# Kernel tuning notes

Measured on AMD Instinct MI355X. Metric: run time of the kernel, lower is better.

## Reference

```python
import jax, jax.numpy as jnp
import numpy as np

LN_EPS = 1e-5

def setup_inputs() -> dict:
    key = jax.random.key(0)
    ks = jax.random.split(key, 5)
    B, S, Dv, Dl, V = 4, 576, 1024, 4096, 32000
    return {
        "vision_feats": jax.random.normal(ks[0], (B, S, Dv), dtype=jnp.float32),
        "W1_w": jax.random.normal(ks[1], (Dl, Dv), dtype=jnp.float32) * (Dv ** -0.5),
        "W1_b": jax.random.normal(ks[2], (Dl,), dtype=jnp.float32) * 0.02,
        "W2_w": jax.random.normal(ks[3], (V, Dl), dtype=jnp.float32) * (Dl ** -0.5),
        "llm_token_embed": jax.random.normal(ks[4], (V, Dl), dtype=jnp.float32) * 0.02,
    }

def reference(vision_feats, W1_w, W1_b, W2_w, llm_token_embed):
    # W1: (B,S,Dv) @ (Dv,Dl) + b -> (B,S,Dl)
    x = jnp.einsum('bsd,ed->bse', vision_feats, W1_w) + W1_b
    # layer_norm over last dim, no affine params
    mu = jnp.mean(x, axis=-1, keepdims=True)
    var = jnp.mean(jnp.square(x - mu), axis=-1, keepdims=True)
    xn = (x - mu) * jax.lax.rsqrt(var + LN_EPS)
    # W2 (no bias): (B,S,Dl) -> (B,S,V) vocab logits
    logits = jnp.einsum('bse,ve->bsv', xn, W2_w)
    P = jax.nn.softmax(logits, axis=-1)
    # softmax-weighted mixture of LLM token embeddings: (B,S,V) @ (V,Dl)
    F_align = jnp.einsum('bsv,ve->bse', P, llm_token_embed)
    return F_align
```

## Files before the change

### kernel.cpp

```cpp
#include <hip/hip_runtime.h>
#include <hip/hip_bf16.h>
#include <stdint.h>

typedef __bf16 bf16_t;
typedef __attribute__((ext_vector_type(8))) __bf16 bf16x8;
typedef __attribute__((ext_vector_type(4))) __bf16 bf16x4;
typedef __attribute__((ext_vector_type(4))) float f32x4;
typedef __attribute__((ext_vector_type(8))) unsigned short u16x8;

#define M_TOK 2304
#define DV    1024
#define DLAT  4096
#define VOCAB 32000

__device__ __forceinline__ float bf2f(unsigned short u) {
  union { unsigned int i; float f; } v; v.i = ((unsigned int)u) << 16; return v.f;
}
__device__ __forceinline__ bf16_t f2bf(float f) { return (bf16_t)f; }

#define GLOAD16(gp, lp) \
  __builtin_amdgcn_global_load_lds( \
      (const __attribute__((address_space(1))) unsigned int*)(const void*)(gp), \
      (__attribute__((address_space(3))) unsigned int*)(void*)(lp), 16, 0, 0)

template<int BN_, int EPI>
__global__ void __launch_bounds__(512, (BN_ == 128 ? 4 : 2))
gemm512(const bf16_t* __restrict__ Ap, const bf16_t* __restrict__ Bp,
        void* __restrict__ Cp, void* __restrict__ Cp2,
        void* __restrict__ Cp3, void* __restrict__ Cp4,
        int Ksplit, int ld, int ldc, int Mt, int Nt)
{
  constexpr int WMR = (BN_ == 128) ? 64 : 128;
  constexpr int NFM = WMR / 16;
  constexpr int LW  = (BN_ == 128) ? 3 : 4;

  __shared__ __align__(16) bf16_t Al[3][256 * 32];
  __shared__ __align__(16) bf16_t Bl[3][BN_ * 32];

  const int nwg = gridDim.x;
  const int orig = blockIdx.x;
  const int q = nwg >> 3, r = nwg & 7;
  const int xcd = orig & 7, idx = orig >> 3;
  const int wg = (xcd < r ? xcd * (q + 1) : r * (q + 1) + (xcd - r) * q) + idx;
  const int mt = wg % Mt;
  const int nt = (wg / Mt) % Nt;
  const int sp = wg / (Mt * Nt);
  const int m0 = mt * 256, n0 = nt * BN_;
  const int kbase = sp * Ksplit;

  const int t    = threadIdx.x;
  const int lane = t & 63, wv = t >> 6;
  const int wm = (BN_ == 128) ? (wv >> 1) : (wv >> 2);
  const int wn = (BN_ == 128) ? (wv & 1)  : (wv & 3);
  const int lr = lane & 15, kc = lane >> 4;

  f32x4 acc[NFM][4];
#pragma unroll
  for (int i = 0; i < NFM; ++i)
#pragma unroll
    for (int j = 0; j < 4; ++j)
#pragma unroll
      for (int x = 0; x < 4; ++x) acc[i][j][x] = 0.0f;

  const int rql = lane >> 2;
  const int cbs = (((lane & 3) ^ ((lane >> 3) & 3)) * 16);
  const int sw8 = (kc ^ ((lr >> 1) & 3)) * 8;
  const size_t rstride = (size_t)ld * 2;

  const int NT = Ksplit / 32;

  auto STAGE = [&](int kt, int nb) {
    const size_t kb = (size_t)(kbase + kt * 32) * 2;
    const char* ga = (const char*)Ap + (size_t)(m0 + wv * 32 + rql) * rstride + kb + cbs;
    char* la = (char*)&Al[nb][0] + wv * 2048;
    GLOAD16(ga, la);
    GLOAD16(ga + 16 * rstride, la + 1024);
    if constexpr (BN_ == 256) {
      const char* gb = (const char*)Bp + (size_t)(n0 + wv * 32 + rql) * rstride + kb + cbs;
      char* lb = (char*)&Bl[nb][0] + wv * 2048;
      GLOAD16(gb, lb);
      GLOAD16(gb + 16 * rstride, lb + 1024);
    } else {
      const char* gb = (const char*)Bp + (size_t)(n0 + wv * 16 + rql) * rstride + kb + cbs;
      char* lb = (char*)&Bl[nb][0] + wv * 1024;
      GLOAD16(gb, lb);
    }
  };

  auto COMPUTE = [&](int nb) {
    bf16x8 af[NFM], bfv[4];
#pragma unroll
    for (int f = 0; f < NFM; ++f)
      af[f] = *(const bf16x8*)(&Al[nb][(wm * WMR + f * 16 + lr) * 32 + sw8]);
#pragma unroll
    for (int f = 0; f < 4; ++f)
      bfv[f] = *(const bf16x8*)(&Bl[nb][(wn * 64 + f * 16 + lr) * 32 + sw8]);
    __builtin_amdgcn_s_setprio(1);
#pragma unroll
    for (int i = 0; i < NFM; ++i)
#pragma unroll
      for (int j = 0; j < 4; ++j)
        acc[i][j] = __builtin_amdgcn_mfma_f32_16x16x32_bf16(af[i], bfv[j], acc[i][j], 0, 0, 0);
    __builtin_amdgcn_s_setprio(0);
  };

  auto WAITL = [&]() {
    if constexpr (LW == 3) asm volatile("s_waitcnt vmcnt(3)" ::: "memory");
    else                   asm volatile("s_waitcnt vmcnt(4)" ::: "memory");
  };
  auto BARX = [&]() {
    asm volatile("s_waitcnt lgkmcnt(0)" ::: "memory");
    __builtin_amdgcn_s_barrier();
  };

  STAGE(0, 0);
  STAGE(1, 1);
  WAITL();
  __builtin_amdgcn_s_barrier();

  int bc = 0, bn = 1, bs = 2;
  for (int kt = 0; kt < NT - 2; ++kt) {
    STAGE(kt + 2, bs);
    COMPUTE(bc);
    WAITL();
    BARX();
    const int tmp = bc; bc = bn; bn = bs; bs = tmp;
  }
  COMPUTE(bc);
  asm volatile("s_waitcnt vmcnt(0)" ::: "memory");
  BARX();
  COMPUTE(bn);

  float* Cf = nullptr;
  if (EPI == 2)
    Cf = (sp == 0) ? (float*)Cp : (sp == 1) ? (float*)Cp2
       : (sp == 2) ? (float*)Cp3 : (float*)Cp4;
#pragma unroll
  for (int j = 0; j < 4; ++j) {
    const int col = n0 + wn * 64 + j * 16 + lr;
#pragma unroll
    for (int i = 0; i < NFM; ++i) {
      const int row = m0 + wm * WMR + i * 16 + kc * 4;
      f32x4 a4 = acc[i][j];
      if (EPI == 1) {
        bf16_t* C = (bf16_t*)Cp;
#pragma unroll
        for (int x = 0; x < 4; ++x) C[(size_t)(row + x) * ldc + col] = f2bf(a4[x]);
      } else {
#pragma unroll
        for (int x = 0; x < 4; ++x) Cf[(size_t)(row + x) * ldc + col] = a4[x];
      }
    }
  }
}

constexpr int GBM = 128, GBN = 128, GBK = 32;

template<int EPI>
__global__ void __launch_bounds__(256, 3)
gemm_bb(const bf16_t* __restrict__ Ap, const bf16_t* __restrict__ Bp,
        void* __restrict__ Cp, const float* __restrict__ bias,
        int K, int ld, int ldc, int Mt)
{
  __shared__ __align__(16) bf16_t Al[3][GBM * GBK];
  __shared__ __align__(16) bf16_t Bl[3][GBN * GBK];

  const int nwg = gridDim.x;
  const int orig = blockIdx.x;
  const int q = nwg >> 3, r = nwg & 7;
  const int xcd = orig & 7, idx = orig >> 3;
  const int wg = (xcd < r ? xcd * (q + 1) : r * (q + 1) + (xcd - r) * q) + idx;
  const int mt = wg % Mt, nt = wg / Mt;
  const int m0 = mt * GBM, n0 = nt * GBN;

  const int t    = threadIdx.x;
  const int lane = t & 63, wv = t >> 6;
  const int wm = wv >> 1, wn = wv & 1;
  const int lr = lane & 15, kc = lane >> 4;

  f32x4 acc[4][4];
#pragma unroll
  for (int i = 0; i < 4; ++i)
#pragma unroll
    for (int j = 0; j < 4; ++j)
#pragma unroll
      for (int x = 0; x < 4; ++x) acc[i][j][x] = 0.0f;

  const int rql = lane >> 2;
  const int cbs = (((lane & 3) ^ ((lane >> 3) & 3)) * 16);
  const int sw8 = (kc ^ ((lr >> 1) & 3)) * 8;
  const size_t rstride = (size_t)ld * 2;

  const int NT = K / GBK;

  auto STAGE = [&](int kt, int nb) {
    const size_t kb = (size_t)kt * GBK * 2;
    const char* ga = (const char*)Ap + (size_t)(m0 + wv * 32 + rql) * rstride + kb + cbs;
    char* la = (char*)&Al[nb][0] + wv * 2048;
    GLOAD16(ga, la);
    GLOAD16(ga + 16 * rstride, la + 1024);
    const char* gb = (const char*)Bp + (size_t)(n0 + wv * 32 + rql) * rstride + kb + cbs;
    char* lb = (char*)&Bl[nb][0] + wv * 2048;
    GLOAD16(gb, lb);
    GLOAD16(gb + 16 * rstride, lb + 1024);
  };

  auto COMPUTE = [&](int nb) {
    bf16x8 af[4], bfv[4];
#pragma unroll
    for (int f = 0; f < 4; ++f)
      af[f] = *(const bf16x8*)(&Al[nb][(wm * 64 + f * 16 + lr) * GBK + sw8]);
#pragma unroll
    for (int f = 0; f < 4; ++f)
      bfv[f] = *(const bf16x8*)(&Bl[nb][(wn * 64 + f * 16 + lr) * GBK + sw8]);
    __builtin_amdgcn_s_setprio(1);
#pragma unroll
    for (int i = 0; i < 4; ++i)
#pragma unroll
      for (int j = 0; j < 4; ++j)
        acc[i][j] = __builtin_amdgcn_mfma_f32_16x16x32_bf16(af[i], bfv[j], acc[i][j], 0, 0, 0);
    __builtin_amdgcn_s_setprio(0);
  };

  auto BARX = [&]() {
    asm volatile("s_waitcnt lgkmcnt(0)" ::: "memory");
    __builtin_amdgcn_s_barrier();
  };

  STAGE(0, 0);
  STAGE(1, 1);
  asm volatile("s_waitcnt vmcnt(4)" ::: "memory");
  __builtin_amdgcn_s_barrier();

  int bc = 0, bn = 1, bs = 2;
  for (int kt = 0; kt < NT - 2; ++kt) {
    STAGE(kt + 2, bs);
    COMPUTE(bc);
    asm volatile("s_waitcnt vmcnt(4)" ::: "memory");
    BARX();
    const int tmp = bc; bc = bn; bn = bs; bs = tmp;
  }
  COMPUTE(bc);
  asm volatile("s_waitcnt vmcnt(0)" ::: "memory");
  BARX();
  COMPUTE(bn);

#pragma unroll
  for (int j = 0; j < 4; ++j) {
    const int col = n0 + wn * 64 + j * 16 + lr;
    const float bv = (EPI == 0) ? bias[col] : 0.0f;
#pragma unroll
    for (int i = 0; i < 4; ++i) {
      const int row = m0 + wm * 64 + i * 16 + kc * 4;
      f32x4 a4 = acc[i][j];
      float* C = (float*)Cp;
#pragma unroll
      for (int x = 0; x < 4; ++x) C[(size_t)(row + x) * ldc + col] = a4[x] + bv;
    }
  }
}

__global__ void __launch_bounds__(256)
addk(float* __restrict__ out, const float* __restrict__ part, int n4)
{
  const int stride = gridDim.x * 256;
  for (int i = blockIdx.x * 256 + threadIdx.x; i < n4; i += stride) {
    f32x4 a = *(const f32x4*)(out + i * 4);
    f32x4 b = *(const f32x4*)(part + i * 4);
#pragma unroll
    for (int x = 0; x < 4; ++x) a[x] += b[x];
    *(f32x4*)(out + i * 4) = a;
  }
}

__global__ void __launch_bounds__(256)
addk3(float* __restrict__ out, const float* __restrict__ pa,
      const float* __restrict__ pb, const float* __restrict__ pc, int n4)
{
  const int stride = gridDim.x * 256;
  for (int i = blockIdx.x * 256 + threadIdx.x; i < n4; i += stride) {
    f32x4 a = *(const f32x4*)(out + i * 4);
    f32x4 b = *(const f32x4*)(pa + i * 4);
    f32x4 c = *(const f32x4*)(pb + i * 4);
    f32x4 d = *(const f32x4*)(pc + i * 4);
#pragma unroll
    for (int x = 0; x < 4; ++x) a[x] += b[x] + c[x] + d[x];
    *(f32x4*)(out + i * 4) = a;
  }
}

__global__ void __launch_bounds__(256)
cvt_bf16_k(const float* __restrict__ in, bf16_t* __restrict__ out, long n8)
{
  const long stride = (long)gridDim.x * 256;
  for (long i = (long)blockIdx.x * 256 + threadIdx.x; i < n8; i += stride) {
    f32x4 a = *(const f32x4*)(in + i * 8);
    f32x4 b = *(const f32x4*)(in + i * 8 + 4);
    bf16x8 o;
#pragma unroll
    for (int j = 0; j < 4; ++j) { o[j] = f2bf(a[j]); o[j + 4] = f2bf(b[j]); }
    *(bf16x8*)(out + i * 8) = o;
  }
}

__global__ void __launch_bounds__(256)
embT_k(const float* __restrict__ E, bf16_t* __restrict__ ET)
{
  __shared__ bf16_t tl[64][72];
  const int vb = blockIdx.x % (VOCAB / 64);
  const int eb = blockIdx.x / (VOCAB / 64);
  const int v0 = vb * 64, e0 = eb * 64;
  const int t = threadIdx.x;

  const int rr = t >> 4, c4 = (t & 15) * 4;
#pragma unroll
  for (int p = 0; p < 4; ++p) {
    const float* src = E + (size_t)(v0 + rr + p * 16) * DLAT + e0 + c4;
    f32x4 a = *(const f32x4*)src;
#pragma unroll
    for (int j = 0; j < 4; ++j) tl[c4 + j][rr + p * 16] = f2bf(a[j]);
  }
  __syncthreads();

  const int el = t >> 3, v8 = (t & 7) * 8;
#pragma unroll
  for (int p = 0; p < 2; ++p) {
    bf16x8 o = *(const bf16x8*)(&tl[el + p * 32][v8]);
    *(bf16x8*)(ET + (size_t)(e0 + el + p * 32) * VOCAB + v0 + v8) = o;
  }
}

__global__ void __launch_bounds__(256)
ln_k(const float* __restrict__ x, bf16_t* __restrict__ xn)
{
  __shared__ float sm[4];
  const int row = blockIdx.x, t = threadIdx.x;
  const float* xr = x + (size_t)row * DLAT;
  f32x4 v[4];
#pragma unroll
  for (int i = 0; i < 4; ++i) v[i] = *(const f32x4*)(xr + (t + i * 256) * 4);

  float s = 0.0f;
#pragma unroll
  for (int i = 0; i < 4; ++i)
#pragma unroll
    for (int j = 0; j < 4; ++j) s += v[i][j];
#pragma unroll
  for (int o = 32; o > 0; o >>= 1) s += __shfl_xor(s, o, 64);
  if ((t & 63) == 0) sm[t >> 6] = s;
  __syncthreads();
  const float mean = (sm[0] + sm[1] + sm[2] + sm[3]) * (1.0f / DLAT);
  __syncthreads();

  float qv = 0.0f;
#pragma unroll
  for (int i = 0; i < 4; ++i)
#pragma unroll
    for (int j = 0; j < 4; ++j) { float d = v[i][j] - mean; qv += d * d; }
#pragma unroll
  for (int o = 32; o > 0; o >>= 1) qv += __shfl_xor(qv, o, 64);
  if ((t & 63) == 0) sm[t >> 6] = qv;
  __syncthreads();
  const float varr = (sm[0] + sm[1] + sm[2] + sm[3]) * (1.0f / DLAT);
  const float rs = rsqrtf(varr + 1e-5f);

  bf16_t* outr = xn + (size_t)row * DLAT;
#pragma unroll
  for (int i = 0; i < 4; ++i) {
    bf16x4 o;
#pragma unroll
    for (int j = 0; j < 4; ++j) o[j] = f2bf((v[i][j] - mean) * rs);
    *(bf16x4*)(outr + (t + i * 256) * 4) = o;
  }
}

__global__ void __launch_bounds__(256)
softmax_k(bf16_t* __restrict__ L)
{
  __shared__ __align__(16) bf16_t rs_[VOCAB];
  __shared__ float sm[4];
  const int row = blockIdx.x, t = threadIdx.x;
  bf16_t* lrow = L + (size_t)row * VOCAB;
  const int NF = VOCAB / 8;

  float m = -3.0e38f;
  for (int f = t; f < NF; f += 256) {
    u16x8 u = *(const u16x8*)(&lrow[f * 8]);
    *(u16x8*)(&rs_[f * 8]) = u;
#pragma unroll
    for (int j = 0; j < 8; ++j) m = fmaxf(m, bf2f(u[j]));
  }
#pragma unroll
  for (int o = 32; o > 0; o >>= 1) m = fmaxf(m, __shfl_xor(m, o, 64));
  if ((t & 63) == 0) sm[t >> 6] = m;
  __syncthreads();
  m = fmaxf(fmaxf(sm[0], sm[1]), fmaxf(sm[2], sm[3]));
  __syncthreads();

  float s = 0.0f;
  for (int f = t; f < NF; f += 256) {
    u16x8 u = *(const u16x8*)(&rs_[f * 8]);
#pragma unroll
    for (int j = 0; j < 8; ++j) s += __expf(bf2f(u[j]) - m);
  }
#pragma unroll
  for (int o = 32; o > 0; o >>= 1) s += __shfl_xor(s, o, 64);
  if ((t & 63) == 0) sm[t >> 6] = s;
  __syncthreads();
  const float inv = 1.0f / (sm[0] + sm[1] + sm[2] + sm[3]);

  for (int f = t; f < NF; f += 256) {
    u16x8 u = *(const u16x8*)(&rs_[f * 8]);
    bf16x8 o;
#pragma unroll
    for (int j = 0; j < 8; ++j) o[j] = f2bf(__expf(bf2f(u[j]) - m) * inv);
    *(bf16x8*)(&lrow[f * 8]) = o;
  }
}

extern "C" void kernel_launch(void* const* d_in, const int* in_sizes, int n_in,
                              void* d_out, int out_size, void* d_ws, size_t ws_size,
                              hipStream_t stream)
{
  (void)in_sizes; (void)n_in; (void)out_size;
  const float* vision = (const float*)d_in[0];
  const float* W1w    = (const float*)d_in[1];
  const float* W1b    = (const float*)d_in[2];
  const float* W2w    = (const float*)d_in[3];
  const float* Emb    = (const float*)d_in[4];
  float* out = (float*)d_out;

  char* ws = (char*)d_ws;
  bf16_t* xn     = (bf16_t*)ws;
  bf16_t* logits = (bf16_t*)(ws + 18874368);
  float*  xbuf   = (float*)(ws + 166330368);
  bf16_t* wslot  = (bf16_t*)(ws + 204079104);
  bf16_t* xnv    = (bf16_t*)(ws + 204079104);
  bf16_t* w1b    = (bf16_t*)(ws + 208797696);
  float*  p2     = (float*)(ws + 466223104);
  float*  p3     = (float*)(ws + 503971840);
  const size_t NEED_BIG = 541720576ull;

  cvt_bf16_k<<<dim3(512), dim3(256), 0, stream>>>(vision, xnv, (long)M_TOK * DV / 8);
  cvt_bf16_k<<<dim3(512), dim3(256), 0, stream>>>(W1w, w1b, (long)DLAT * DV / 8);

  gemm_bb<0><<<dim3(18 * 32), dim3(256), 0, stream>>>(
      xnv, w1b, xbuf, W1b, DV, DV, DLAT, 18);

  ln_k<<<dim3(M_TOK), dim3(256), 0, stream>>>(xbuf, xn);

  cvt_bf16_k<<<dim3(2048), dim3(256), 0, stream>>>(W2w, wslot, (long)VOCAB * DLAT / 8);

  gemm512<256, 1><<<dim3(9 * 125), dim3(512), 0, stream>>>(
      xn, wslot, logits, nullptr, nullptr, nullptr, DLAT, DLAT, VOCAB, 9, 125);

  embT_k<<<dim3((VOCAB / 64) * (DLAT / 64)), dim3(256), 0, stream>>>(Emb, wslot);

  softmax_k<<<dim3(M_TOK), dim3(256), 0, stream>>>(logits);

  if (ws_size >= NEED_BIG) {
    gemm512<256, 2><<<dim3(9 * 16 * 4), dim3(512), 0, stream>>>(
        logits, wslot, out, xbuf, p2, p3, VOCAB / 4, VOCAB, DLAT, 9, 16);
    addk3<<<dim3(1024), dim3(256), 0, stream>>>(out, xbuf, p2, p3, (M_TOK * DLAT) / 4);
  } else {
    gemm512<128, 2><<<dim3(9 * 32 * 2), dim3(512), 0, stream>>>(
        logits, wslot, out, xbuf, nullptr, nullptr, VOCAB / 2, VOCAB, DLAT, 9, 32);
    addk<<<dim3(1024), dim3(256), 0, stream>>>(out, xbuf, (M_TOK * DLAT) / 4);
  }
}
```

Before: 2.301 ms.

## Replace 512-thread GEMM with 256-thread 256x128 tile kernel, 64x128 per wave

Replaces the 512-thread 256x256 (or 256x128) block GEMM with a 256-thread kernel using 256x128 tiles, where each of four waves computes a 64x128 sub-tile (4x8 MFMA fragments). Both the logits GEMM and the split-K mixture GEMM now use this kernel, with the grids doubled along N to match. Larger per-wave tiles raise MFMA work per LDS fragment load, at the cost of more accumulator registers (128 floats) and a B tile half the size of before for the big path.

After: 1.991 ms. 13.5% less time.

```diff
diff --git a/kernel.cpp b/kernel.cpp
--- a/kernel.cpp
+++ b/kernel.cpp
@@ -23,19 +23,15 @@
       (const __attribute__((address_space(1))) unsigned int*)(const void*)(gp), \
       (__attribute__((address_space(3))) unsigned int*)(void*)(lp), 16, 0, 0)
 
-template<int BN_, int EPI>
-__global__ void __launch_bounds__(512, (BN_ == 128 ? 4 : 2))
-gemm512(const bf16_t* __restrict__ Ap, const bf16_t* __restrict__ Bp,
-        void* __restrict__ Cp, void* __restrict__ Cp2,
-        void* __restrict__ Cp3, void* __restrict__ Cp4,
-        int Ksplit, int ld, int ldc, int Mt, int Nt)
-{
-  constexpr int WMR = (BN_ == 128) ? 64 : 128;
-  constexpr int NFM = WMR / 16;
-  constexpr int LW  = (BN_ == 128) ? 3 : 4;
-
+template<int EPI>
+__global__ void __launch_bounds__(256, 2)
+gemm256r(const bf16_t* __restrict__ Ap, const bf16_t* __restrict__ Bp,
+         void* __restrict__ Cp, void* __restrict__ Cp2,
+         void* __restrict__ Cp3, void* __restrict__ Cp4,
+         int Ksplit, int ld, int ldc, int Mt, int Nt)
+{
   __shared__ __align__(16) bf16_t Al[3][256 * 32];
-  __shared__ __align__(16) bf16_t Bl[3][BN_ * 32];
+  __shared__ __align__(16) bf16_t Bl[3][128 * 32];
 
   const int nwg = gridDim.x;
   const int orig = blockIdx.x;
@@ -45,20 +41,18 @@
   const int mt = wg % Mt;
   const int nt = (wg / Mt) % Nt;
   const int sp = wg / (Mt * Nt);
-  const int m0 = mt * 256, n0 = nt * BN_;
+  const int m0 = mt * 256, n0 = nt * 128;
   const int kbase = sp * Ksplit;
 
   const int t    = threadIdx.x;
   const int lane = t & 63, wv = t >> 6;
-  const int wm = (BN_ == 128) ? (wv >> 1) : (wv >> 2);
-  const int wn = (BN_ == 128) ? (wv & 1)  : (wv & 3);
   const int lr = lane & 15, kc = lane >> 4;
 
-  f32x4 acc[NFM][4];
-#pragma unroll
-  for (int i = 0; i < NFM; ++i)
-#pragma unroll
-    for (int j = 0; j < 4; ++j)
+  f32x4 acc[4][8];
+#pragma unroll
+  for (int i = 0; i < 4; ++i)
+#pragma unroll
+    for (int j = 0; j < 8; ++j)
 #pragma unroll
       for (int x = 0; x < 4; ++x) acc[i][j][x] = 0.0f;
 
@@ -71,43 +65,35 @@
 
   auto STAGE = [&](int kt, int nb) {
     const size_t kb = (size_t)(kbase + kt * 32) * 2;
-    const char* ga = (const char*)Ap + (size_t)(m0 + wv * 32 + rql) * rstride + kb + cbs;
-    char* la = (char*)&Al[nb][0] + wv * 2048;
+    const char* ga = (const char*)Ap + (size_t)(m0 + wv * 64 + rql) * rstride + kb + cbs;
+    char* la = (char*)&Al[nb][0] + wv * 4096;
     GLOAD16(ga, la);
     GLOAD16(ga + 16 * rstride, la + 1024);
-    if constexpr (BN_ == 256) {
-      const char* gb = (const char*)Bp + (size_t)(n0 + wv * 32 + rql) * rstride + kb + cbs;
-      char* lb = (char*)&Bl[nb][0] + wv * 2048;
-      GLOAD16(gb, lb);
-      GLOAD16(gb + 16 * rstride, lb + 1024);
-    } else {
-      const char* gb = (const char*)Bp + (size_t)(n0 + wv * 16 + rql) * rstride + kb + cbs;
-      char* lb = (char*)&Bl[nb][0] + wv * 1024;
-      GLOAD16(gb, lb);
-    }
+    GLOAD16(ga + 32 * rstride, la + 2048);
+    GLOAD16(ga + 48 * rstride, la + 3072);
+    const char* gb = (const char*)Bp + (size_t)(n0 + wv * 32 + rql) * rstride + kb + cbs;
+    char* lb = (char*)&Bl[nb][0] + wv * 2048;
+    GLOAD16(gb, lb);
+    GLOAD16(gb + 16 * rstride, lb + 1024);
   };
 
   auto COMPUTE = [&](int nb) {
-    bf16x8 af[NFM], bfv[4];
-#pragma unroll
-    for (int f = 0; f < NFM; ++f)
-      af[f] = *(const bf16x8*)(&Al[nb][(wm * WMR + f * 16 + lr) * 32 + sw8]);
+    bf16x8 af[4], bfv[8];
 #pragma unroll
     for (int f = 0; f < 4; ++f)
-      bfv[f] = *(const bf16x8*)(&Bl[nb][(wn * 64 + f * 16 + lr) * 32 + sw8]);
+      af[f] = *(const bf16x8*)(&Al[nb][(wv * 64 + f * 16 + lr) * 32 + sw8]);
+#pragma unroll
+    for (int f = 0; f < 8; ++f)
+      bfv[f] = *(const bf16x8*)(&Bl[nb][(f * 16 + lr) * 32 + sw8]);
     __builtin_amdgcn_s_setprio(1);
 #pragma unroll
-    for (int i = 0; i < NFM; ++i)
-#pragma unroll
-      for (int j = 0; j < 4; ++j)
+    for (int i = 0; i < 4; ++i)
+#pragma unroll
+      for (int j = 0; j < 8; ++j)
         acc[i][j] = __builtin_amdgcn_mfma_f32_16x16x32_bf16(af[i], bfv[j], acc[i][j], 0, 0, 0);
     __builtin_amdgcn_s_setprio(0);
   };
 
-  auto WAITL = [&]() {
-    if constexpr (LW == 3) asm volatile("s_waitcnt vmcnt(3)" ::: "memory");
-    else                   asm volatile("s_waitcnt vmcnt(4)" ::: "memory");
-  };
   auto BARX = [&]() {
     asm volatile("s_waitcnt lgkmcnt(0)" ::: "memory");
     __builtin_amdgcn_s_barrier();
@@ -115,14 +101,14 @@
 
   STAGE(0, 0);
   STAGE(1, 1);
-  WAITL();
+  asm volatile("s_waitcnt vmcnt(6)" ::: "memory");
   __builtin_amdgcn_s_barrier();
 
   int bc = 0, bn = 1, bs = 2;
   for (int kt = 0; kt < NT - 2; ++kt) {
     STAGE(kt + 2, bs);
     COMPUTE(bc);
-    WAITL();
+    asm volatile("s_waitcnt vmcnt(6)" ::: "memory");
     BARX();
     const int tmp = bc; bc = bn; bn = bs; bs = tmp;
   }
@@ -136,11 +122,11 @@
     Cf = (sp == 0) ? (float*)Cp : (sp == 1) ? (float*)Cp2
        : (sp == 2) ? (float*)Cp3 : (float*)Cp4;
 #pragma unroll
-  for (int j = 0; j < 4; ++j) {
-    const int col = n0 + wn * 64 + j * 16 + lr;
-#pragma unroll
-    for (int i = 0; i < NFM; ++i) {
-      const int row = m0 + wm * WMR + i * 16 + kc * 4;
+  for (int j = 0; j < 8; ++j) {
+    const int col = n0 + j * 16 + lr;
+#pragma unroll
+    for (int i = 0; i < 4; ++i) {
+      const int row = m0 + wv * 64 + i * 16 + kc * 4;
       f32x4 a4 = acc[i][j];
       if (EPI == 1) {
         bf16_t* C = (bf16_t*)Cp;
@@ -156,11 +142,10 @@
 
 constexpr int GBM = 128, GBN = 128, GBK = 32;
 
-template<int EPI>
 __global__ void __launch_bounds__(256, 3)
-gemm_bb(const bf16_t* __restrict__ Ap, const bf16_t* __restrict__ Bp,
-        void* __restrict__ Cp, const float* __restrict__ bias,
-        int K, int ld, int ldc, int Mt)
+gemm_bb1(const bf16_t* __restrict__ Ap, const bf16_t* __restrict__ Bp,
+         float* __restrict__ Cp, const float* __restrict__ bias,
+         int K, int ld, int ldc, int Mt)
 {
   __shared__ __align__(16) bf16_t Al[3][GBM * GBK];
   __shared__ __align__(16) bf16_t Bl[3][GBN * GBK];
@@ -248,28 +233,14 @@
 #pragma unroll
   for (int j = 0; j < 4; ++j) {
     const int col = n0 + wn * 64 + j * 16 + lr;
-    const float bv = (EPI == 0) ? bias[col] : 0.0f;
+    const float bv = bias[col];
 #pragma unroll
     for (int i = 0; i < 4; ++i) {
       const int row = m0 + wm * 64 + i * 16 + kc * 4;
       f32x4 a4 = acc[i][j];
-      float* C = (float*)Cp;
-#pragma unroll
-      for (int x = 0; x < 4; ++x) C[(size_t)(row + x) * ldc + col] = a4[x] + bv;
+#pragma unroll
+      for (int x = 0; x < 4; ++x) Cp[(size_t)(row + x) * ldc + col] = a4[x] + bv;
     }
-  }
-}
-
-__global__ void __launch_bounds__(256)
-addk(float* __restrict__ out, const float* __restrict__ part, int n4)
-{
-  const int stride = gridDim.x * 256;
-  for (int i = blockIdx.x * 256 + threadIdx.x; i < n4; i += stride) {
-    f32x4 a = *(const f32x4*)(out + i * 4);
-    f32x4 b = *(const f32x4*)(part + i * 4);
-#pragma unroll
-    for (int x = 0; x < 4; ++x) a[x] += b[x];
-    *(f32x4*)(out + i * 4) = a;
   }
 }
 
@@ -285,6 +256,19 @@
     f32x4 d = *(const f32x4*)(pc + i * 4);
 #pragma unroll
     for (int x = 0; x < 4; ++x) a[x] += b[x] + c[x] + d[x];
+    *(f32x4*)(out + i * 4) = a;
+  }
+}
+
+__global__ void __launch_bounds__(256)
+addk(float* __restrict__ out, const float* __restrict__ part, int n4)
+{
+  const int stride = gridDim.x * 256;
+  for (int i = blockIdx.x * 256 + threadIdx.x; i < n4; i += stride) {
+    f32x4 a = *(const f32x4*)(out + i * 4);
+    f32x4 b = *(const f32x4*)(part + i * 4);
+#pragma unroll
+    for (int x = 0; x < 4; ++x) a[x] += b[x];
     *(f32x4*)(out + i * 4) = a;
   }
 }
@@ -439,31 +423,31 @@
   bf16_t* w1b    = (bf16_t*)(ws + 208797696);
   float*  p2     = (float*)(ws + 466223104);
   float*  p3     = (float*)(ws + 503971840);
-  const size_t NEED_BIG = 541720576ull;
+  const size_t NEED4 = 541720576ull;
 
   cvt_bf16_k<<<dim3(512), dim3(256), 0, stream>>>(vision, xnv, (long)M_TOK * DV / 8);
   cvt_bf16_k<<<dim3(512), dim3(256), 0, stream>>>(W1w, w1b, (long)DLAT * DV / 8);
 
-  gemm_bb<0><<<dim3(18 * 32), dim3(256), 0, stream>>>(
+  gemm_bb1<<<dim3(18 * 32), dim3(256), 0, stream>>>(
       xnv, w1b, xbuf, W1b, DV, DV, DLAT, 18);
 
   ln_k<<<dim3(M_TOK), dim3(256), 0, stream>>>(xbuf, xn);
 
   cvt_bf16_k<<<dim3(2048), dim3(256), 0, stream>>>(W2w, wslot, (long)VOCAB * DLAT / 8);
 
-  gemm512<256, 1><<<dim3(9 * 125), dim3(512), 0, stream>>>(
-      xn, wslot, logits, nullptr, nullptr, nullptr, DLAT, DLAT, VOCAB, 9, 125);
+  gemm256r<1><<<dim3(9 * 250), dim3(256), 0, stream>>>(
+      xn, wslot, logits, nullptr, nullptr, nullptr, DLAT, DLAT, VOCAB, 9, 250);
 
   embT_k<<<dim3((VOCAB / 64) * (DLAT / 64)), dim3(256), 0, stream>>>(Emb, wslot);
 
   softmax_k<<<dim3(M_TOK), dim3(256), 0, stream>>>(logits);
 
-  if (ws_size >= NEED_BIG) {
-    gemm512<256, 2><<<dim3(9 * 16 * 4), dim3(512), 0, stream>>>(
-        logits, wslot, out, xbuf, p2, p3, VOCAB / 4, VOCAB, DLAT, 9, 16);
+  if (ws_size >= NEED4) {
+    gemm256r<2><<<dim3(9 * 32 * 4), dim3(256), 0, stream>>>(
+        logits, wslot, out, xbuf, p2, p3, VOCAB / 4, VOCAB, DLAT, 9, 32);
     addk3<<<dim3(1024), dim3(256), 0, stream>>>(out, xbuf, p2, p3, (M_TOK * DLAT) / 4);
   } else {
-    gemm512<128, 2><<<dim3(9 * 32 * 2), dim3(512), 0, stream>>>(
+    gemm256r<2><<<dim3(9 * 32 * 2), dim3(256), 0, stream>>>(
         logits, wslot, out, xbuf, nullptr, nullptr, VOCAB / 2, VOCAB, DLAT, 9, 32);
     addk<<<dim3(1024), dim3(256), 0, stream>>>(out, xbuf, (M_TOK * DLAT) / 4);
   }
```
